# Kernel tuning notes

Measured on AMD Instinct MI355X. Metric: run time of the kernel, lower is better.

The kernel has to match this reference:

```python
import jax, jax.numpy as jnp
import numpy as np

IN_F = 4096
OUT_F = 4096
RANK = 16
ALPHA = 32
BLOCK = 64  # quantization blocksize along in_features
SCALING = ALPHA / RANK


def setup_inputs() -> dict:
    key = jax.random.key(0)
    k1, k2, k3, k4, k5, k6 = jax.random.split(key, 6)
    x = jax.random.normal(k1, (4, 2048, IN_F), dtype=jnp.float32)
    # int4 codes stored with +8 offset, values in [0, 16)
    q_codes = jax.random.randint(k2, (OUT_F, IN_F), 0, 16, dtype=jnp.int32)
    # per-(row, block) dequant scales
    scales = jax.random.uniform(k3, (OUT_F, IN_F // BLOCK), dtype=jnp.float32) * 0.02
    bias = jax.random.normal(k4, (OUT_F,), dtype=jnp.float32) * 0.02
    lora_A = jax.random.normal(k5, (RANK, IN_F), dtype=jnp.float32) * (1.0 / np.sqrt(IN_F))
    lora_B = jax.random.normal(k6, (OUT_F, RANK), dtype=jnp.float32) * 0.02
    return {"x": x, "q_codes": q_codes, "scales": scales, "bias": bias,
            "lora_A": lora_A, "lora_B": lora_B}


def _dequant(q_codes, scales):
    # [O, I] int4 codes (offset by 8) -> fp32 weight via blockwise scales
    O, I = q_codes.shape
    c = (q_codes.astype(jnp.float32) - 8.0).reshape(O, I // BLOCK, BLOCK)
    return (c * scales[:, :, None]).reshape(O, I)


def reference(x, q_codes, scales, bias, lora_A, lora_B):
    w = _dequant(q_codes, scales)                      # [O, I]
    base = jnp.einsum('bsi,oi->bso', x, w) + bias      # dequant GEMM + bias
    # LoRA branch: dropout(p=0) is identity; x @ (B@A).T == (x @ A.T) @ B.T
    lora = jnp.einsum('bsr,or->bso', jnp.einsum('bsi,ri->bsr', x, lora_A), lora_B)
    return base + lora * SCALING
```

## Files before the change

kernel.cpp:

```cpp
#include <hip/hip_runtime.h>
#include <hip/hip_bf16.h>

#define IN_F   4096
#define OUT_F  4096
#define RANK   16
#define M_TOK  8192
#define SCALING 2.0f

typedef __attribute__((ext_vector_type(8))) short short8;
typedef __attribute__((ext_vector_type(4))) float f32x4;
typedef __attribute__((ext_vector_type(4))) float fvec4;
typedef __attribute__((ext_vector_type(4))) int   ivec4;
typedef __attribute__((ext_vector_type(4))) unsigned int uvec4;

__global__ __launch_bounds__(256) void prep2(const float* __restrict__ x,
                                             __hip_bfloat16* __restrict__ xb,
                                             const int* __restrict__ q,
                                             const float* __restrict__ sc,
                                             const float* __restrict__ lA,
                                             const float* __restrict__ lB,
                                             __hip_bfloat16* __restrict__ W) {
    const int bid = blockIdx.x;
    const int tid = threadIdx.x;
    if (bid & 1) {
        const size_t base   = (size_t)(bid >> 1) * 256 + tid;
        const size_t stride = (size_t)2048 * 256;
#pragma unroll
        for (int it = 0; it < 8; ++it) {
            const size_t i = (base + (size_t)it * stride) * 8;
            fvec4 a = __builtin_nontemporal_load((const fvec4*)(x + i));
            fvec4 b = __builtin_nontemporal_load((const fvec4*)(x + i + 4));
            union { uvec4 u; __hip_bfloat16 h[8]; } p;
            p.h[0] = __float2bfloat16(a.x);
            p.h[1] = __float2bfloat16(a.y);
            p.h[2] = __float2bfloat16(a.z);
            p.h[3] = __float2bfloat16(a.w);
            p.h[4] = __float2bfloat16(b.x);
            p.h[5] = __float2bfloat16(b.y);
            p.h[6] = __float2bfloat16(b.z);
            p.h[7] = __float2bfloat16(b.w);
            *(uvec4*)(xb + i) = p.u;
        }
    } else {
        const int id = bid >> 1;
        const int c0 = (id & 3) * 1024 + tid * 4;
        const int o0 = (id >> 2) * 8;

        ivec4 qv[8];
#pragma unroll
        for (int oo = 0; oo < 8; ++oo)
            qv[oo] = __builtin_nontemporal_load(
                (const ivec4*)(q + (size_t)(o0 + oo) * IN_F + c0));

        float sv[8];
#pragma unroll
        for (int oo = 0; oo < 8; ++oo)
            sv[oo] = sc[(o0 + oo) * (IN_F / 64) + (c0 >> 6)];

        fvec4 a[RANK];
#pragma unroll
        for (int r = 0; r < RANK; ++r)
            a[r] = *(const fvec4*)(lA + (size_t)r * IN_F + c0);

#pragma unroll
        for (int oo = 0; oo < 8; ++oo) {
            const float* lbo = lB + (size_t)(o0 + oo) * RANK;
            float l0 = 0.f, l1 = 0.f, l2 = 0.f, l3 = 0.f;
#pragma unroll
            for (int r = 0; r < RANK; ++r) {
                const float br = lbo[r];
                l0 += br * a[r].x; l1 += br * a[r].y;
                l2 += br * a[r].z; l3 += br * a[r].w;
            }
            const float s = sv[oo];
            union { ushort4 u; __hip_bfloat16 h[4]; } p;
            p.h[0] = __float2bfloat16((float)(qv[oo].x - 8) * s + SCALING * l0);
            p.h[1] = __float2bfloat16((float)(qv[oo].y - 8) * s + SCALING * l1);
            p.h[2] = __float2bfloat16((float)(qv[oo].z - 8) * s + SCALING * l2);
            p.h[3] = __float2bfloat16((float)(qv[oo].w - 8) * s + SCALING * l3);
            *(ushort4*)(W + (size_t)(o0 + oo) * IN_F + c0) = p.u;
        }
    }
}


__device__ __forceinline__ void load_lds16(const void* g, void* l) {
    __builtin_amdgcn_global_load_lds(
        (const __attribute__((address_space(1))) unsigned int*)g,
        (__attribute__((address_space(3))) unsigned int*)l, 16, 0, 0);
}

#define MFMA_BF16 __builtin_amdgcn_mfma_f32_16x16x32_bf16

__global__ __launch_bounds__(512, 2) void gemm256_8ph(const __hip_bfloat16* __restrict__ A,
                                                      const __hip_bfloat16* __restrict__ B,
                                                      const float* __restrict__ bias,
                                                      float* __restrict__ C) {
    extern __shared__ __align__(16) char lds[];

    const int tid  = threadIdx.x;
    const int lane = tid & 63;
    const int wave = tid >> 6;

    const int xcd = blockIdx.x & 7;
    const int w64 = blockIdx.x >> 3;
    const int tm  = (xcd >> 1) * 8 + (w64 >> 3);
    const int tn  = (xcd & 1) * 8 + (w64 & 7);

    const __hip_bfloat16* Ab = A + (size_t)tm * 256 * IN_F;
    const __hip_bfloat16* Bb = B + (size_t)tn * 256 * IN_F;

    const int    c0   = ((lane & 3) * 8) ^ ((lane >= 32) ? 16 : 0);
    const size_t off0 = (size_t)((wave >> 1) * 16 + (lane >> 2)) * IN_F
                      + (size_t)((wave & 1) * 32 + c0);

    const __hip_bfloat16* qA0 = Ab + off0;
    const __hip_bfloat16* qA1 = Ab + (size_t)128 * IN_F + off0;
    const __hip_bfloat16* qB0 = Bb + off0;
    const __hip_bfloat16* qB1 = Bb + (size_t)128 * IN_F + off0;

    const int flo = (lane & 15) * 64 + (((lane >> 4) * 16) ^ ((lane & 8) << 2));

    const int ah = wave >> 2;
    const int bh = (wave >> 1) & 1;
    const int bs = (wave & 1) * 4;

    const char* aRd[2] = { lds + ah * 16384 + flo,
                           lds + 65536 + ah * 16384 + flo };
    const char* bRd[2] = { lds + 32768 + bh * 16384 + bs * 2048 + flo,
                           lds + 65536 + 32768 + bh * 16384 + bs * 2048 + flo };

    const int wv1024 = wave * 1024;

#define STAGE2(ps, te, LO) do {                                             \
        const __hip_bfloat16* g_ = (ps) + (te);                             \
        load_lds16(g_,              lds + (LO) + wv1024);                   \
        load_lds16(g_ + 64 * IN_F,  lds + (LO) + 8192 + wv1024);            \
    } while (0)

    STAGE2(qB0, 0,  32768);
    STAGE2(qB1, 0,  49152);
    STAGE2(qA0, 0,  0);
    STAGE2(qA1, 0,  16384);
    STAGE2(qB0, 64, 65536 + 32768);
    STAGE2(qB1, 64, 65536 + 49152);
    asm volatile("s_waitcnt vmcnt(4)" ::: "memory");
    __builtin_amdgcn_s_barrier();

    short8 aF[4][2], bAf[2][2], bBf[2][2];
    f32x4 acc[8][4] = {};

#define TILE(T, CBI) do {                                                          \
        const int t1e = (((T) + 1) & 63) << 6;        \
        const int t2e = (((T) + 2) & 63) << 6;                                     \
                           \
        _Pragma("unroll")                                                          \
        for (int i = 0; i < 4; ++i)                                                \
            _Pragma("unroll")                                                      \
            for (int kk = 0; kk < 2; ++kk)                                         \
                aF[i][kk] = *(const short8*)(aRd[CBI] + (i * 2 + kk) * 1024);      \
        _Pragma("unroll")                                                          \
        for (int j = 0; j < 2; ++j)                                                \
            _Pragma("unroll")                                                      \
            for (int kk = 0; kk < 2; ++kk)                                         \
                bAf[j][kk] = *(const short8*)(bRd[CBI] + (j * 2 + kk) * 1024);     \
        STAGE2(qA0, t1e, ((CBI) ^ 1) * 65536);                                     \
        __builtin_amdgcn_s_barrier();                                              \
        __builtin_amdgcn_s_setprio(1);                                             \
        _Pragma("unroll")                                                          \
        for (int i = 0; i < 4; ++i)                                                \
            _Pragma("unroll")                                                      \
            for (int j = 0; j < 2; ++j)                                            \
                _Pragma("unroll")                                                  \
                for (int kk = 0; kk < 2; ++kk)                                     \
                    acc[i][j] = MFMA_BF16(aF[i][kk], bAf[j][kk], acc[i][j], 0,0,0);\
        __builtin_amdgcn_s_setprio(0);                                             \
        __builtin_amdgcn_s_barrier();                                              \
                           \
        _Pragma("unroll")                                                          \
        for (int j = 0; j < 2; ++j)                                                \
            _Pragma("unroll")                                                      \
            for (int kk = 0; kk < 2; ++kk)                                         \
                bBf[j][kk] = *(const short8*)(bRd[CBI] + 4096 + (j*2+kk) * 1024);  \
        STAGE2(qA1, t1e, ((CBI) ^ 1) * 65536 + 16384);                             \
        __builtin_amdgcn_s_barrier();                                              \
        __builtin_amdgcn_s_setprio(1);                                             \
        _Pragma("unroll")                                                          \
        for (int i = 0; i < 4; ++i)                                                \
            _Pragma("unroll")                                                      \
            for (int j = 0; j < 2; ++j)                                            \
                _Pragma("unroll")                                                  \
                for (int kk = 0; kk < 2; ++kk)                                     \
                    acc[i][2+j] = MFMA_BF16(aF[i][kk], bBf[j][kk], acc[i][2+j],0,0,0);\
        __builtin_amdgcn_s_setprio(0);                                             \
        __builtin_amdgcn_s_barrier();                                              \
                           \
        _Pragma("unroll")                                                          \
        for (int i = 0; i < 4; ++i)                                                \
            _Pragma("unroll")                                                      \
            for (int kk = 0; kk < 2; ++kk)                                         \
                aF[i][kk] = *(const short8*)(aRd[CBI] + 8192 + (i*2+kk) * 1024);   \
        STAGE2(qB0, t2e, (CBI) * 65536 + 32768);               \
        __builtin_amdgcn_s_barrier();                                              \
        __builtin_amdgcn_s_setprio(1);                                             \
        _Pragma("unroll")                                                          \
        for (int i = 0; i < 4; ++i)                                                \
            _Pragma("unroll")                                                      \
            for (int j = 0; j < 2; ++j)                                            \
                _Pragma("unroll")                                                  \
                for (int kk = 0; kk < 2; ++kk)                                     \
                    acc[4+i][2+j] = MFMA_BF16(aF[i][kk], bBf[j][kk], acc[4+i][2+j],0,0,0);\
        __builtin_amdgcn_s_setprio(0);                                             \
        __builtin_amdgcn_s_barrier();                                              \
                           \
        STAGE2(qB1, t2e, (CBI) * 65536 + 49152);                                   \
        asm volatile("s_waitcnt vmcnt(4)" ::: "memory");      \
        __builtin_amdgcn_s_barrier();                          \
        __builtin_amdgcn_s_setprio(1);                                             \
        _Pragma("unroll")                                                          \
        for (int i = 0; i < 4; ++i)                                                \
            _Pragma("unroll")                                                      \
            for (int j = 0; j < 2; ++j)                                            \
                _Pragma("unroll")                                                  \
                for (int kk = 0; kk < 2; ++kk)                                     \
                    acc[4+i][j] = MFMA_BF16(aF[i][kk], bAf[j][kk], acc[4+i][j],0,0,0);\
        __builtin_amdgcn_s_setprio(0);                                             \
        __builtin_amdgcn_s_barrier();                                              \
    } while (0)

    for (int tt = 0; tt < 32; ++tt) {
        TILE(2 * tt,     0);
        TILE(2 * tt + 1, 1);
    }
    asm volatile("s_waitcnt vmcnt(0)" ::: "memory");

    const int qd = lane >> 4;
    const int cl = lane & 15;
    const size_t m_base = (size_t)tm * 256 + (size_t)ah * 128;
    const int    n_base = tn * 256 + (wave & 3) * 64;
#pragma unroll
    for (int fn = 0; fn < 4; ++fn) {
        const int n = n_base + fn * 16 + cl;
        const float bv = bias[n];
#pragma unroll
        for (int fm = 0; fm < 8; ++fm) {
            const size_t m0 = m_base + fm * 16 + qd * 4;
#pragma unroll
            for (int r = 0; r < 4; ++r)
                __builtin_nontemporal_store(acc[fm][fn][r] + bv,
                                            &C[(m0 + r) * OUT_F + n]);
        }
    }
#undef STAGE2
#undef TILE
}

extern "C" void kernel_launch(void* const* d_in, const int* in_sizes, int n_in,
                              void* d_out, int out_size, void* d_ws, size_t ws_size,
                              hipStream_t stream) {
    const float* x    = (const float*)d_in[0];
    const int*   qc   = (const int*)d_in[1];
    const float* sc   = (const float*)d_in[2];
    const float* bias = (const float*)d_in[3];
    const float* lA   = (const float*)d_in[4];
    const float* lB   = (const float*)d_in[5];
    float* out = (float*)d_out;

    __hip_bfloat16* xb = (__hip_bfloat16*)d_ws;
    __hip_bfloat16* wb = xb + (size_t)M_TOK * IN_F;

    static bool attr_done = false;
    if (!attr_done) {
        (void)hipFuncSetAttribute((const void*)gemm256_8ph,
                                  hipFuncAttributeMaxDynamicSharedMemorySize, 131072);
        attr_done = true;
    }

    prep2<<<4096, 256, 0, stream>>>(x, xb, qc, sc, lA, lB, wb);
    gemm256_8ph<<<dim3(512), dim3(512), 131072, stream>>>(xb, wb, bias, out);
}
```

Before: 486.1 us.

## Fuse fp32-to-bf16 conversion of x into the GEMM A-operand load path

Removes the separate pass that converted x to bf16 in workspace. The GEMM now loads fp32 x straight into registers, converts to bf16 and writes it to LDS with ds stores, replacing the async global_load_lds for the A tile. This saves writing and rereading a bf16 copy of x, but it doubles the A-tile global read bytes, since every column tile of the GEMM rereads fp32 x. It also adds register pressure and extra LDS-write waits inside the pipelined main loop.

```diff
diff --git a/kernel.cpp b/kernel.cpp
--- a/kernel.cpp
+++ b/kernel.cpp
@@ -13,73 +13,49 @@
 typedef __attribute__((ext_vector_type(4))) int   ivec4;
 typedef __attribute__((ext_vector_type(4))) unsigned int uvec4;
 
-__global__ __launch_bounds__(256) void prep2(const float* __restrict__ x,
-                                             __hip_bfloat16* __restrict__ xb,
-                                             const int* __restrict__ q,
-                                             const float* __restrict__ sc,
-                                             const float* __restrict__ lA,
-                                             const float* __restrict__ lB,
-                                             __hip_bfloat16* __restrict__ W) {
-    const int bid = blockIdx.x;
+__global__ __launch_bounds__(256) void dequant_lora(const int* __restrict__ q,
+                                                    const float* __restrict__ sc,
+                                                    const float* __restrict__ lA,
+                                                    const float* __restrict__ lB,
+                                                    __hip_bfloat16* __restrict__ W) {
     const int tid = threadIdx.x;
-    if (bid & 1) {
-        const size_t base   = (size_t)(bid >> 1) * 256 + tid;
-        const size_t stride = (size_t)2048 * 256;
-#pragma unroll
-        for (int it = 0; it < 8; ++it) {
-            const size_t i = (base + (size_t)it * stride) * 8;
-            fvec4 a = __builtin_nontemporal_load((const fvec4*)(x + i));
-            fvec4 b = __builtin_nontemporal_load((const fvec4*)(x + i + 4));
-            union { uvec4 u; __hip_bfloat16 h[8]; } p;
-            p.h[0] = __float2bfloat16(a.x);
-            p.h[1] = __float2bfloat16(a.y);
-            p.h[2] = __float2bfloat16(a.z);
-            p.h[3] = __float2bfloat16(a.w);
-            p.h[4] = __float2bfloat16(b.x);
-            p.h[5] = __float2bfloat16(b.y);
-            p.h[6] = __float2bfloat16(b.z);
-            p.h[7] = __float2bfloat16(b.w);
-            *(uvec4*)(xb + i) = p.u;
+    const int id  = blockIdx.x;
+    const int c0  = (id & 3) * 1024 + tid * 4;
+    const int o0  = (id >> 2) * 8;
+
+    ivec4 qv[8];
+#pragma unroll
+    for (int oo = 0; oo < 8; ++oo)
+        qv[oo] = __builtin_nontemporal_load(
+            (const ivec4*)(q + (size_t)(o0 + oo) * IN_F + c0));
+
+    float sv[8];
+#pragma unroll
+    for (int oo = 0; oo < 8; ++oo)
+        sv[oo] = sc[(o0 + oo) * (IN_F / 64) + (c0 >> 6)];
+
+    fvec4 a[RANK];
+#pragma unroll
+    for (int r = 0; r < RANK; ++r)
+        a[r] = *(const fvec4*)(lA + (size_t)r * IN_F + c0);
+
+#pragma unroll
+    for (int oo = 0; oo < 8; ++oo) {
+        const float* lbo = lB + (size_t)(o0 + oo) * RANK;
+        float l0 = 0.f, l1 = 0.f, l2 = 0.f, l3 = 0.f;
+#pragma unroll
+        for (int r = 0; r < RANK; ++r) {
+            const float br = lbo[r];
+            l0 += br * a[r].x; l1 += br * a[r].y;
+            l2 += br * a[r].z; l3 += br * a[r].w;
         }
-    } else {
-        const int id = bid >> 1;
-        const int c0 = (id & 3) * 1024 + tid * 4;
-        const int o0 = (id >> 2) * 8;
-
-        ivec4 qv[8];
-#pragma unroll
-        for (int oo = 0; oo < 8; ++oo)
-            qv[oo] = __builtin_nontemporal_load(
-                (const ivec4*)(q + (size_t)(o0 + oo) * IN_F + c0));
-
-        float sv[8];
-#pragma unroll
-        for (int oo = 0; oo < 8; ++oo)
-            sv[oo] = sc[(o0 + oo) * (IN_F / 64) + (c0 >> 6)];
-
-        fvec4 a[RANK];
-#pragma unroll
-        for (int r = 0; r < RANK; ++r)
-            a[r] = *(const fvec4*)(lA + (size_t)r * IN_F + c0);
-
-#pragma unroll
-        for (int oo = 0; oo < 8; ++oo) {
-            const float* lbo = lB + (size_t)(o0 + oo) * RANK;
-            float l0 = 0.f, l1 = 0.f, l2 = 0.f, l3 = 0.f;
-#pragma unroll
-            for (int r = 0; r < RANK; ++r) {
-                const float br = lbo[r];
-                l0 += br * a[r].x; l1 += br * a[r].y;
-                l2 += br * a[r].z; l3 += br * a[r].w;
-            }
-            const float s = sv[oo];
-            union { ushort4 u; __hip_bfloat16 h[4]; } p;
-            p.h[0] = __float2bfloat16((float)(qv[oo].x - 8) * s + SCALING * l0);
-            p.h[1] = __float2bfloat16((float)(qv[oo].y - 8) * s + SCALING * l1);
-            p.h[2] = __float2bfloat16((float)(qv[oo].z - 8) * s + SCALING * l2);
-            p.h[3] = __float2bfloat16((float)(qv[oo].w - 8) * s + SCALING * l3);
-            *(ushort4*)(W + (size_t)(o0 + oo) * IN_F + c0) = p.u;
-        }
+        const float s = sv[oo];
+        union { ushort4 u; __hip_bfloat16 h[4]; } p;
+        p.h[0] = __float2bfloat16((float)(qv[oo].x - 8) * s + SCALING * l0);
+        p.h[1] = __float2bfloat16((float)(qv[oo].y - 8) * s + SCALING * l1);
+        p.h[2] = __float2bfloat16((float)(qv[oo].z - 8) * s + SCALING * l2);
+        p.h[3] = __float2bfloat16((float)(qv[oo].w - 8) * s + SCALING * l3);
+        *(ushort4*)(W + (size_t)(o0 + oo) * IN_F + c0) = p.u;
     }
 }
 
@@ -92,7 +68,7 @@
 
 #define MFMA_BF16 __builtin_amdgcn_mfma_f32_16x16x32_bf16
 
-__global__ __launch_bounds__(512, 2) void gemm256_8ph(const __hip_bfloat16* __restrict__ A,
+__global__ __launch_bounds__(512, 2) void gemm256_8ph(const float* __restrict__ X,
                                                       const __hip_bfloat16* __restrict__ B,
                                                       const float* __restrict__ bias,
                                                       float* __restrict__ C) {
@@ -107,15 +83,14 @@
     const int tm  = (xcd >> 1) * 8 + (w64 >> 3);
     const int tn  = (xcd & 1) * 8 + (w64 & 7);
 
-    const __hip_bfloat16* Ab = A + (size_t)tm * 256 * IN_F;
     const __hip_bfloat16* Bb = B + (size_t)tn * 256 * IN_F;
 
-    const int    c0   = ((lane & 3) * 8) ^ ((lane >= 32) ? 16 : 0);
-    const size_t off0 = (size_t)((wave >> 1) * 16 + (lane >> 2)) * IN_F
-                      + (size_t)((wave & 1) * 32 + c0);
-
-    const __hip_bfloat16* qA0 = Ab + off0;
-    const __hip_bfloat16* qA1 = Ab + (size_t)128 * IN_F + off0;
+    const int c0   = ((lane & 3) * 8) ^ ((lane >= 32) ? 16 : 0);
+    const int arow = (wave >> 1) * 16 + (lane >> 2);
+    const int acol = (wave & 1) * 32 + c0;
+
+    const float* xA = X + (size_t)(tm * 256 + arow) * IN_F + acol;
+    const size_t off0 = (size_t)arow * IN_F + acol;
     const __hip_bfloat16* qB0 = Bb + off0;
     const __hip_bfloat16* qB1 = Bb + (size_t)128 * IN_F + off0;
 
@@ -130,7 +105,28 @@
     const char* bRd[2] = { lds + 32768 + bh * 16384 + bs * 2048 + flo,
                            lds + 65536 + 32768 + bh * 16384 + bs * 2048 + flo };
 
-    const int wv1024 = wave * 1024;
+    const int wv1024 = wave * 1024 + lane * 16;
+
+    f32x4 aR[4][2];
+
+#define ALOAD(SLOT, TE) do {                                                \
+        const float* p_ = xA + (size_t)(SLOT) * 64 * IN_F + (TE);           \
+        aR[SLOT][0] = *(const f32x4*)(p_);                                  \
+        aR[SLOT][1] = *(const f32x4*)(p_ + 4);                              \
+    } while (0)
+
+#define ASTORE(SLOT, NB) do {                                               \
+        union { __hip_bfloat16 h[8]; uvec4 v; } pk_;                        \
+        pk_.h[0] = __float2bfloat16(aR[SLOT][0].x);                         \
+        pk_.h[1] = __float2bfloat16(aR[SLOT][0].y);                         \
+        pk_.h[2] = __float2bfloat16(aR[SLOT][0].z);                         \
+        pk_.h[3] = __float2bfloat16(aR[SLOT][0].w);                         \
+        pk_.h[4] = __float2bfloat16(aR[SLOT][1].x);                         \
+        pk_.h[5] = __float2bfloat16(aR[SLOT][1].y);                         \
+        pk_.h[6] = __float2bfloat16(aR[SLOT][1].z);                         \
+        pk_.h[7] = __float2bfloat16(aR[SLOT][1].w);                         \
+        *(uvec4*)(lds + (NB) + (SLOT) * 8192 + wv1024) = pk_.v;             \
+    } while (0)
 
 #define STAGE2(ps, te, LO) do {                                             \
         const __hip_bfloat16* g_ = (ps) + (te);                             \
@@ -138,13 +134,14 @@
         load_lds16(g_ + 64 * IN_F,  lds + (LO) + 8192 + wv1024);            \
     } while (0)
 
+    ALOAD(0, 0); ALOAD(1, 0); ALOAD(2, 0); ALOAD(3, 0);
     STAGE2(qB0, 0,  32768);
     STAGE2(qB1, 0,  49152);
-    STAGE2(qA0, 0,  0);
-    STAGE2(qA1, 0,  16384);
     STAGE2(qB0, 64, 65536 + 32768);
     STAGE2(qB1, 64, 65536 + 49152);
     asm volatile("s_waitcnt vmcnt(4)" ::: "memory");
+    ASTORE(0, 0); ASTORE(1, 0); ASTORE(2, 0); ASTORE(3, 0);
+    asm volatile("s_waitcnt lgkmcnt(0)" ::: "memory");
     __builtin_amdgcn_s_barrier();
 
     short8 aF[4][2], bAf[2][2], bBf[2][2];
@@ -164,7 +161,7 @@
             _Pragma("unroll")                                                      \
             for (int kk = 0; kk < 2; ++kk)                                         \
                 bAf[j][kk] = *(const short8*)(bRd[CBI] + (j * 2 + kk) * 1024);     \
-        STAGE2(qA0, t1e, ((CBI) ^ 1) * 65536);                                     \
+        ALOAD(0, t1e); ALOAD(1, t1e);                                              \
         __builtin_amdgcn_s_barrier();                                              \
         __builtin_amdgcn_s_setprio(1);                                             \
         _Pragma("unroll")                                                          \
@@ -182,7 +179,7 @@
             _Pragma("unroll")                                                      \
             for (int kk = 0; kk < 2; ++kk)                                         \
                 bBf[j][kk] = *(const short8*)(bRd[CBI] + 4096 + (j*2+kk) * 1024);  \
-        STAGE2(qA1, t1e, ((CBI) ^ 1) * 65536 + 16384);                             \
+        ALOAD(2, t1e); ALOAD(3, t1e);                                              \
         __builtin_amdgcn_s_barrier();                                              \
         __builtin_amdgcn_s_setprio(1);                                             \
         _Pragma("unroll")                                                          \
@@ -214,7 +211,7 @@
         __builtin_amdgcn_s_barrier();                                              \
                            \
         STAGE2(qB1, t2e, (CBI) * 65536 + 49152);                                   \
-        asm volatile("s_waitcnt vmcnt(4)" ::: "memory");      \
+        asm volatile("s_waitcnt vmcnt(4)" ::: "memory");     \
         __builtin_amdgcn_s_barrier();                          \
         __builtin_amdgcn_s_setprio(1);                                             \
         _Pragma("unroll")                                                          \
@@ -225,6 +222,10 @@
                 for (int kk = 0; kk < 2; ++kk)                                     \
                     acc[4+i][j] = MFMA_BF16(aF[i][kk], bAf[j][kk], acc[4+i][j],0,0,0);\
         __builtin_amdgcn_s_setprio(0);                                             \
+               \
+        ASTORE(0, ((CBI)^1) * 65536); ASTORE(1, ((CBI)^1) * 65536);                \
+        ASTORE(2, ((CBI)^1) * 65536); ASTORE(3, ((CBI)^1) * 65536);                \
+        asm volatile("s_waitcnt lgkmcnt(0)" ::: "memory");     \
         __builtin_amdgcn_s_barrier();                                              \
     } while (0)
 
@@ -253,6 +254,8 @@
     }
 #undef STAGE2
 #undef TILE
+#undef ALOAD
+#undef ASTORE
 }
 
 extern "C" void kernel_launch(void* const* d_in, const int* in_sizes, int n_in,
@@ -266,8 +269,7 @@
     const float* lB   = (const float*)d_in[5];
     float* out = (float*)d_out;
 
-    __hip_bfloat16* xb = (__hip_bfloat16*)d_ws;
-    __hip_bfloat16* wb = xb + (size_t)M_TOK * IN_F;
+    __hip_bfloat16* wb = (__hip_bfloat16*)d_ws;
 
     static bool attr_done = false;
     if (!attr_done) {
@@ -276,6 +278,6 @@
         attr_done = true;
     }
 
-    prep2<<<4096, 256, 0, stream>>>(x, xb, qc, sc, lA, lB, wb);
-    gemm256_8ph<<<dim3(512), dim3(512), 131072, stream>>>(xb, wb, bias, out);
-}
+    dequant_lora<<<2048, 256, 0, stream>>>(qc, sc, lA, lB, wb);
+    gemm256_8ph<<<dim3(512), dim3(512), 131072, stream>>>(x, wb, bias, out);
+}
```

New measurement: 529.8 us. 1.09x slower.

## Prefetch both GEMM operands two tiles ahead and split prep kernel

Applied to the files above, without the earlier changes.

The GEMM main loop now issues the A-operand LDS loads for tile T+2 in the last phase of tile T, instead of loading A one tile ahead during the early phases. All B and A stages are grouped, and the wait depth is raised to vmcnt(8), so more global-to-LDS traffic stays in flight behind the MFMA work. Separately, the fused prep kernel is split into an x-to-bf16 conversion kernel and a dequant+LoRA kernel. That adds one launch, and the two prep tasks no longer interleave within a single grid.

```diff
diff --git a/kernel.cpp b/kernel.cpp
--- a/kernel.cpp
+++ b/kernel.cpp
@@ -13,73 +13,70 @@
 typedef __attribute__((ext_vector_type(4))) int   ivec4;
 typedef __attribute__((ext_vector_type(4))) unsigned int uvec4;
 
-__global__ __launch_bounds__(256) void prep2(const float* __restrict__ x,
-                                             __hip_bfloat16* __restrict__ xb,
-                                             const int* __restrict__ q,
-                                             const float* __restrict__ sc,
-                                             const float* __restrict__ lA,
-                                             const float* __restrict__ lB,
-                                             __hip_bfloat16* __restrict__ W) {
-    const int bid = blockIdx.x;
+__global__ __launch_bounds__(256) void cvt_x(const float* __restrict__ x,
+                                             __hip_bfloat16* __restrict__ xb) {
+    const size_t nvec = (size_t)M_TOK * IN_F / 8;
+    const size_t stride = (size_t)gridDim.x * 256;
+    for (size_t idx = (size_t)blockIdx.x * 256 + threadIdx.x; idx < nvec; idx += stride) {
+        const size_t i = idx * 8;
+        fvec4 a = __builtin_nontemporal_load((const fvec4*)(x + i));
+        fvec4 b = __builtin_nontemporal_load((const fvec4*)(x + i + 4));
+        union { uvec4 u; __hip_bfloat16 h[8]; } p;
+        p.h[0] = __float2bfloat16(a.x);
+        p.h[1] = __float2bfloat16(a.y);
+        p.h[2] = __float2bfloat16(a.z);
+        p.h[3] = __float2bfloat16(a.w);
+        p.h[4] = __float2bfloat16(b.x);
+        p.h[5] = __float2bfloat16(b.y);
+        p.h[6] = __float2bfloat16(b.z);
+        p.h[7] = __float2bfloat16(b.w);
+        *(uvec4*)(xb + i) = p.u;
+    }
+}
+
+__global__ __launch_bounds__(256) void dequant_lora(const int* __restrict__ q,
+                                                    const float* __restrict__ sc,
+                                                    const float* __restrict__ lA,
+                                                    const float* __restrict__ lB,
+                                                    __hip_bfloat16* __restrict__ W) {
     const int tid = threadIdx.x;
-    if (bid & 1) {
-        const size_t base   = (size_t)(bid >> 1) * 256 + tid;
-        const size_t stride = (size_t)2048 * 256;
-#pragma unroll
-        for (int it = 0; it < 8; ++it) {
-            const size_t i = (base + (size_t)it * stride) * 8;
-            fvec4 a = __builtin_nontemporal_load((const fvec4*)(x + i));
-            fvec4 b = __builtin_nontemporal_load((const fvec4*)(x + i + 4));
-            union { uvec4 u; __hip_bfloat16 h[8]; } p;
-            p.h[0] = __float2bfloat16(a.x);
-            p.h[1] = __float2bfloat16(a.y);
-            p.h[2] = __float2bfloat16(a.z);
-            p.h[3] = __float2bfloat16(a.w);
-            p.h[4] = __float2bfloat16(b.x);
-            p.h[5] = __float2bfloat16(b.y);
-            p.h[6] = __float2bfloat16(b.z);
-            p.h[7] = __float2bfloat16(b.w);
-            *(uvec4*)(xb + i) = p.u;
+    const int id  = blockIdx.x;
+    const int c0  = (id & 3) * 1024 + tid * 4;
+    const int o0  = (id >> 2) * 8;
+
+    ivec4 qv[8];
+#pragma unroll
+    for (int oo = 0; oo < 8; ++oo)
+        qv[oo] = __builtin_nontemporal_load(
+            (const ivec4*)(q + (size_t)(o0 + oo) * IN_F + c0));
+
+    float sv[8];
+#pragma unroll
+    for (int oo = 0; oo < 8; ++oo)
+        sv[oo] = sc[(o0 + oo) * (IN_F / 64) + (c0 >> 6)];
+
+    fvec4 a[RANK];
+#pragma unroll
+    for (int r = 0; r < RANK; ++r)
+        a[r] = *(const fvec4*)(lA + (size_t)r * IN_F + c0);
+
+#pragma unroll
+    for (int oo = 0; oo < 8; ++oo) {
+        const float* lbo = lB + (size_t)(o0 + oo) * RANK;
+        float l0 = 0.f, l1 = 0.f, l2 = 0.f, l3 = 0.f;
+#pragma unroll
+        for (int r = 0; r < RANK; ++r) {
+            const float br = lbo[r];
+            l0 += br * a[r].x; l1 += br * a[r].y;
+            l2 += br * a[r].z; l3 += br * a[r].w;
         }
-    } else {
-        const int id = bid >> 1;
-        const int c0 = (id & 3) * 1024 + tid * 4;
-        const int o0 = (id >> 2) * 8;
-
-        ivec4 qv[8];
-#pragma unroll
-        for (int oo = 0; oo < 8; ++oo)
-            qv[oo] = __builtin_nontemporal_load(
-                (const ivec4*)(q + (size_t)(o0 + oo) * IN_F + c0));
-
-        float sv[8];
-#pragma unroll
-        for (int oo = 0; oo < 8; ++oo)
-            sv[oo] = sc[(o0 + oo) * (IN_F / 64) + (c0 >> 6)];
-
-        fvec4 a[RANK];
-#pragma unroll
-        for (int r = 0; r < RANK; ++r)
-            a[r] = *(const fvec4*)(lA + (size_t)r * IN_F + c0);
-
-#pragma unroll
-        for (int oo = 0; oo < 8; ++oo) {
-            const float* lbo = lB + (size_t)(o0 + oo) * RANK;
-            float l0 = 0.f, l1 = 0.f, l2 = 0.f, l3 = 0.f;
-#pragma unroll
-            for (int r = 0; r < RANK; ++r) {
-                const float br = lbo[r];
-                l0 += br * a[r].x; l1 += br * a[r].y;
-                l2 += br * a[r].z; l3 += br * a[r].w;
-            }
-            const float s = sv[oo];
-            union { ushort4 u; __hip_bfloat16 h[4]; } p;
-            p.h[0] = __float2bfloat16((float)(qv[oo].x - 8) * s + SCALING * l0);
-            p.h[1] = __float2bfloat16((float)(qv[oo].y - 8) * s + SCALING * l1);
-            p.h[2] = __float2bfloat16((float)(qv[oo].z - 8) * s + SCALING * l2);
-            p.h[3] = __float2bfloat16((float)(qv[oo].w - 8) * s + SCALING * l3);
-            *(ushort4*)(W + (size_t)(o0 + oo) * IN_F + c0) = p.u;
-        }
+        const float s = sv[oo];
+        union { ushort4 u; __hip_bfloat16 h[4]; } p;
+        p.h[0] = __float2bfloat16((float)(qv[oo].x - 8) * s + SCALING * l0);
+        p.h[1] = __float2bfloat16((float)(qv[oo].y - 8) * s + SCALING * l1);
+        p.h[2] = __float2bfloat16((float)(qv[oo].z - 8) * s + SCALING * l2);
+        p.h[3] = __float2bfloat16((float)(qv[oo].w - 8) * s + SCALING * l3);
+        *(ushort4*)(W + (size_t)(o0 + oo) * IN_F + c0) = p.u;
     }
 }
 
@@ -144,15 +141,16 @@
     STAGE2(qA1, 0,  16384);
     STAGE2(qB0, 64, 65536 + 32768);
     STAGE2(qB1, 64, 65536 + 49152);
-    asm volatile("s_waitcnt vmcnt(4)" ::: "memory");
+    STAGE2(qA0, 64, 65536 + 0);
+    STAGE2(qA1, 64, 65536 + 16384);
+    asm volatile("s_waitcnt vmcnt(8)" ::: "memory");
     __builtin_amdgcn_s_barrier();
 
     short8 aF[4][2], bAf[2][2], bBf[2][2];
     f32x4 acc[8][4] = {};
 
 #define TILE(T, CBI) do {                                                          \
-        const int t1e = (((T) + 1) & 63) << 6;        \
-        const int t2e = (((T) + 2) & 63) << 6;                                     \
+        const int t2e = (((T) + 2) & 63) << 6;        \
                            \
         _Pragma("unroll")                                                          \
         for (int i = 0; i < 4; ++i)                                                \
@@ -164,7 +162,6 @@
             _Pragma("unroll")                                                      \
             for (int kk = 0; kk < 2; ++kk)                                         \
                 bAf[j][kk] = *(const short8*)(bRd[CBI] + (j * 2 + kk) * 1024);     \
-        STAGE2(qA0, t1e, ((CBI) ^ 1) * 65536);                                     \
         __builtin_amdgcn_s_barrier();                                              \
         __builtin_amdgcn_s_setprio(1);                                             \
         _Pragma("unroll")                                                          \
@@ -182,7 +179,6 @@
             _Pragma("unroll")                                                      \
             for (int kk = 0; kk < 2; ++kk)                                         \
                 bBf[j][kk] = *(const short8*)(bRd[CBI] + 4096 + (j*2+kk) * 1024);  \
-        STAGE2(qA1, t1e, ((CBI) ^ 1) * 65536 + 16384);                             \
         __builtin_amdgcn_s_barrier();                                              \
         __builtin_amdgcn_s_setprio(1);                                             \
         _Pragma("unroll")                                                          \
@@ -200,7 +196,8 @@
             _Pragma("unroll")                                                      \
             for (int kk = 0; kk < 2; ++kk)                                         \
                 aF[i][kk] = *(const short8*)(aRd[CBI] + 8192 + (i*2+kk) * 1024);   \
-        STAGE2(qB0, t2e, (CBI) * 65536 + 32768);               \
+        STAGE2(qB0, t2e, (CBI) * 65536 + 32768);          \
+        STAGE2(qB1, t2e, (CBI) * 65536 + 49152);                                   \
         __builtin_amdgcn_s_barrier();                                              \
         __builtin_amdgcn_s_setprio(1);                                             \
         _Pragma("unroll")                                                          \
@@ -213,8 +210,9 @@
         __builtin_amdgcn_s_setprio(0);                                             \
         __builtin_amdgcn_s_barrier();                                              \
                            \
-        STAGE2(qB1, t2e, (CBI) * 65536 + 49152);                                   \
-        asm volatile("s_waitcnt vmcnt(4)" ::: "memory");      \
+        STAGE2(qA0, t2e, (CBI) * 65536 + 0);              \
+        STAGE2(qA1, t2e, (CBI) * 65536 + 16384);                                   \
+        asm volatile("s_waitcnt vmcnt(8)" ::: "memory");      \
         __builtin_amdgcn_s_barrier();                          \
         __builtin_amdgcn_s_setprio(1);                                             \
         _Pragma("unroll")                                                          \
@@ -276,6 +274,7 @@
         attr_done = true;
     }
 
-    prep2<<<4096, 256, 0, stream>>>(x, xb, qc, sc, lA, lB, wb);
+    cvt_x<<<2048, 256, 0, stream>>>(x, xb);
+    dequant_lora<<<2048, 256, 0, stream>>>(qc, sc, lA, lB, wb);
     gemm256_8ph<<<dim3(512), dim3(512), 131072, stream>>>(xb, wb, bias, out);
 }
```

After: 489.5 us. Within noise of the previous version (+0.7%).
